# Kernel optimization log

Hardware: AMD Instinct MI355X
Metric: run time of the kernel (lower is better)

The kernel has to match this reference:

```python
import jax, jax.numpy as jnp
import numpy as np

NEG = -9.0e15


def setup_inputs() -> dict:
    key = jax.random.key(0)
    k_x, k_w, k_e, k_b, k_m = jax.random.split(key, 5)
    B, N, C, F = 2048, 64, 256, 256
    x = jax.random.normal(k_x, (B, N, C), dtype=jnp.float32)
    W = jax.random.normal(k_w, (2, C, F), dtype=jnp.float32) * (1.414 / np.sqrt(C + F))
    # full logit tensor; only entries where mask holds are ever read (equivalent
    # to torch's flat `e` scattered into the nonzero positions of adj)
    e = jax.random.normal(k_e, (F, N, N), dtype=jnp.float32)
    bias = jax.random.normal(k_b, (F,), dtype=jnp.float32) * (1.0 / np.sqrt(C))
    # symmetric adjacency mask with self-loops, density ~0.3
    m = jax.random.bernoulli(k_m, 0.3, (N, N))
    mask = (m | m.T) | jnp.eye(N, dtype=bool)
    return {"x": x, "W": W, "e": e, "bias": bias, "mask": mask}


def reference(x, W, e, bias, mask):
    # x: [B,N,C], W: [2,C,F], e: [F,N,N], bias: [F], mask: [N,N] bool
    h0 = x @ W[0]                                   # [B,N,F] (self term)
    h1 = x @ W[1]                                   # [B,N,F] (neighbor term)
    logits = jnp.where(mask[None, :, :], e, NEG)    # [F,N,N]
    adj = jax.nn.softmax(logits, axis=2)            # per-channel row softmax
    N = mask.shape[0]
    eye = jnp.eye(N, dtype=bool)
    d = jnp.diagonal(adj, axis1=1, axis2=2)         # [F,N]  (adj * E diagonal)
    off = jnp.where(eye[None, :, :], 0.0, adj)      # [F,N,N] (adj * (1-E))
    # (adj*E) @ h0 reduces to per-node diagonal scaling; off-diag is a
    # per-channel NxN matmul batched over B.
    out = d.T[None, :, :] * h0 + jnp.einsum('fnm,bmf->bnf', off, h1)
    return out + bias[None, None, :]
```

## Files before the change

kernel.cpp:

```cpp
#include <hip/hip_runtime.h>
#include <hip/hip_bf16.h>


typedef __attribute__((ext_vector_type(8))) short  fragA;
typedef __attribute__((ext_vector_type(4))) float  f32x4;
typedef __attribute__((ext_vector_type(8))) unsigned short u16x8;
typedef __attribute__((ext_vector_type(4))) unsigned short u16x4;

constexpr long OFF_OFF = 0;
constexpr long OFF_WT  = 2l * 1024 * 1024;
constexpr long OFF_DS  = OFF_WT + 512l * 256 * 2;
constexpr long WS_NEED = OFF_DS + 64l * 256 * 4;

static __device__ inline unsigned short f2bf(float f) {
  __hip_bfloat16 h = __float2bfloat16(f);
  return __builtin_bit_cast(unsigned short, h);
}
static __device__ inline float bf2f(unsigned short u) {
  unsigned int x = ((unsigned int)u) << 16;
  return __builtin_bit_cast(float, x);
}

__global__ __launch_bounds__(256) void k_prep(const float* __restrict__ e,
                                              const unsigned char* __restrict__ mask,
                                              char* __restrict__ ws_b) {
  unsigned short* off = (unsigned short*)(ws_b + OFF_OFF);
  float* dscale = (float*)(ws_b + OFF_DS);
  const int lane = threadIdx.x & 63;
  const int row  = blockIdx.x * 4 + (threadIdx.x >> 6);
  const int n = row & 63;

  bool is_u8 = __all(mask[lane * 65] != 0);
  bool mv;
  if (is_u8) mv = mask[n * 64 + lane] != 0;
  else       mv = ((const int*)mask)[n * 64 + lane] != 0;

  float v = mv ? e[(long)row * 64 + lane] : -1e30f;
  float mx = v;
#pragma unroll
  for (int s = 32; s; s >>= 1) mx = fmaxf(mx, __shfl_xor(mx, s));
  float ex = mv ? __expf(v - mx) : 0.f;
  float sm = ex;
#pragma unroll
  for (int s = 32; s; s >>= 1) sm += __shfl_xor(sm, s);
  float adj = ex / sm;
  const int f = row >> 6;
  if (lane == n) dscale[n * 256 + f] = adj;
  off[(long)row * 64 + lane] = f2bf(lane == n ? 0.f : adj);
}

__global__ __launch_bounds__(256) void k_wt(const float* __restrict__ W,
                                            char* __restrict__ ws_b) {
  unsigned short* Wt = (unsigned short*)(ws_b + OFF_WT);
  __shared__ float t[64][65];
  const int bid = blockIdx.x;
  const int w = bid >> 4, f0 = ((bid >> 2) & 3) * 64, c0 = (bid & 3) * 64;
  const int tr = threadIdx.x >> 2, tc = (threadIdx.x & 3) * 16;
  const float* src = W + ((long)(w * 256 + c0 + tr)) * 256 + f0 + tc;
#pragma unroll
  for (int i = 0; i < 16; i += 4) {
    float4 v = *(const float4*)(src + i);
    t[tr][tc + i] = v.x; t[tr][tc + i + 1] = v.y;
    t[tr][tc + i + 2] = v.z; t[tr][tc + i + 3] = v.w;
  }
  __syncthreads();
  u16x8 p0, p1;
#pragma unroll
  for (int i = 0; i < 8; i++)  p0[i] = f2bf(t[tc + i][tr]);
#pragma unroll
  for (int i = 0; i < 8; i++)  p1[i] = f2bf(t[tc + 8 + i][tr]);
  unsigned short* dst = Wt + ((long)(w * 256 + f0 + tr)) * 256 + c0 + tc;
  *(u16x8*)dst = p0;
  *(u16x8*)(dst + 8) = p1;
}

__global__ __launch_bounds__(512, 4) void k_main(const float* __restrict__ x,
                                                 const float* __restrict__ bias,
                                                 const char* __restrict__ ws_b,
                                                 float* __restrict__ out) {
  const unsigned short* Wt   = (const unsigned short*)(ws_b + OFF_WT);
  const unsigned short* offp = (const unsigned short*)(ws_b + OFF_OFF);
  const float* dscale        = (const float*)(ws_b + OFF_DS);

  __shared__ __align__(16) unsigned short Bs[64 * 264];
  __shared__ __align__(16) unsigned short Hb[19264];

  const int tid = threadIdx.x;
  const int wid = tid >> 6, lane = tid & 63;
  const int lr = lane & 15, hi = lane >> 4;

  const int wg = blockIdx.x;
  const int xcd = wg & 7, s = wg >> 3;
  const int bb = xcd * 32 + (s >> 3);
  const int fb = s & 7;
  const int f0 = fb * 32;
  const long R0 = (long)bb * 512;
  const long Rw = R0 + wid * 64;

  {
    int c = tid >> 3, ch = (tid & 7) * 32;
    int wrow = (c < 32) ? (f0 + c) : (256 + f0 + c - 32);
    const unsigned short* src = Wt + (long)wrow * 256 + ch;
    unsigned short* d = &Bs[c * 264 + ch];
    *(u16x8*)(d)      = *(const u16x8*)(src);
    *(u16x8*)(d + 8)  = *(const u16x8*)(src + 8);
    *(u16x8*)(d + 16) = *(const u16x8*)(src + 16);
    *(u16x8*)(d + 24) = *(const u16x8*)(src + 24);
  }
  __syncthreads();

  f32x4 acc[4][4] = {};
#pragma unroll
  for (int ks = 0; ks < 8; ks++) {
    fragA af[4], bfr[4];
#pragma unroll
    for (int i = 0; i < 4; i++) {
      const float* p = x + (Rw + i * 16 + lr) * 256 + ks * 32 + hi * 8;
      float4 v0 = *(const float4*)p;
      float4 v1 = *(const float4*)(p + 4);
      u16x8 t;
      t[0] = f2bf(v0.x); t[1] = f2bf(v0.y); t[2] = f2bf(v0.z); t[3] = f2bf(v0.w);
      t[4] = f2bf(v1.x); t[5] = f2bf(v1.y); t[6] = f2bf(v1.z); t[7] = f2bf(v1.w);
      af[i] = __builtin_bit_cast(fragA, t);
    }
#pragma unroll
    for (int j = 0; j < 4; j++)
      bfr[j] = *(const fragA*)&Bs[(j * 16 + lr) * 264 + ks * 32 + hi * 8];
#pragma unroll
    for (int i = 0; i < 4; i++)
#pragma unroll
      for (int j = 0; j < 4; j++)
        acc[i][j] = __builtin_amdgcn_mfma_f32_16x16x32_bf16(af[i], bfr[j], acc[i][j], 0, 0, 0);
  }

#pragma unroll
  for (int i = 0; i < 4; i++) {
#pragma unroll
    for (int j = 2; j < 4; j++) {
      int fl = (j - 2) * 16 + lr;
      int m  = i * 16 + hi * 4;
      u16x4 pk;
      pk[0] = f2bf(acc[i][j][0]); pk[1] = f2bf(acc[i][j][1]);
      pk[2] = f2bf(acc[i][j][2]); pk[3] = f2bf(acc[i][j][3]);
      *(u16x4*)&Hb[fl * 584 + wid * 72 + m] = pk;
    }
  }
  __syncthreads();

#pragma unroll
  for (int q = 0; q < 4; q++) {
    int fl = wid * 4 + q;
    long fg = f0 + fl;
    f32x4 ea[4] = {};
    const unsigned short* ob = offp + fg * 4096;
#pragma unroll
    for (int kk = 0; kk < 2; kk++) {
      fragA a = *(const fragA*)&Hb[fl * 584 + lr * 72 + kk * 32 + hi * 8];
#pragma unroll
      for (int ct = 0; ct < 4; ct++) {
        fragA b = *(const fragA*)(ob + (ct * 16 + lr) * 64 + kk * 32 + hi * 8);
        ea[ct] = __builtin_amdgcn_mfma_f32_16x16x32_bf16(a, b, ea[ct], 0, 0, 0);
      }
    }
    if (hi < 2) {
#pragma unroll
      for (int ct = 0; ct < 4; ct++) {
#pragma unroll
        for (int r = 0; r < 4; r++) {
          int b = hi * 4 + r;
          int n = ct * 16 + lr;
          Hb[fl * 584 + b * 72 + n] = f2bf(ea[ct][r]);
        }
      }
    }
  }
  __syncthreads();

#pragma unroll
  for (int i = 0; i < 4; i++) {
#pragma unroll
    for (int j = 0; j < 2; j++) {
      int fl = j * 16 + lr;
      int f  = f0 + fl;
      float bs = bias[f];
#pragma unroll
      for (int r = 0; r < 4; r++) {
        int m = i * 16 + hi * 4 + r;
        float ev = bf2f(Hb[fl * 584 + wid * 72 + m]);
        long R = Rw + m;
        out[R * 256 + f] = dscale[m * 256 + f] * acc[i][j][r] + ev + bs;
      }
    }
  }
}

extern "C" void kernel_launch(void* const* d_in, const int* in_sizes, int n_in,
                              void* d_out, int out_size, void* d_ws, size_t ws_size,
                              hipStream_t stream) {
  const float* x    = (const float*)d_in[0];
  const float* W    = (const float*)d_in[1];
  const float* e    = (const float*)d_in[2];
  const float* bias = (const float*)d_in[3];
  const unsigned char* mask = (const unsigned char*)d_in[4];
  float* out = (float*)d_out;
  char* ws = (char*)d_ws;
  if (ws_size < (size_t)WS_NEED) return;

  k_prep<<<4096, 256, 0, stream>>>(e, mask, ws);
  k_wt<<<32, 256, 0, stream>>>(W, ws);
  k_main<<<2048, 512, 0, stream>>>(x, bias, ws, out);
}
```

Before: 205.5 us.

## Pre-convert x to bf16 in a fused prep kernel and prefetch A fragments

Adds a bf16 copy of x in workspace, produced by a single merged prep kernel that also computes the softmax adjacency and transposed weights. The main kernel now reads bf16 x with register double-buffered prefetch, uses 256-thread blocks over twice as many row tiles, and the per-channel neighbor matmul uses only the needed rows. This removes in-loop fp32 loads and conversions and one launch, but adds an extra full pass writing and rereading x in bf16.

```diff
diff --git a/kernel.cpp b/kernel.cpp
--- a/kernel.cpp
+++ b/kernel.cpp
@@ -10,7 +10,8 @@
 constexpr long OFF_OFF = 0;
 constexpr long OFF_WT  = 2l * 1024 * 1024;
 constexpr long OFF_DS  = OFF_WT + 512l * 256 * 2;
-constexpr long WS_NEED = OFF_DS + 64l * 256 * 4;
+constexpr long OFF_XB  = OFF_DS + 64l * 256 * 4;
+constexpr long WS_NEED = OFF_XB + 131072l * 256 * 2;
 
 static __device__ inline unsigned short f2bf(float f) {
   __hip_bfloat16 h = __float2bfloat16(f);
@@ -21,116 +22,130 @@
   return __builtin_bit_cast(float, x);
 }
 
-__global__ __launch_bounds__(256) void k_prep(const float* __restrict__ e,
-                                              const unsigned char* __restrict__ mask,
-                                              char* __restrict__ ws_b) {
-  unsigned short* off = (unsigned short*)(ws_b + OFF_OFF);
-  float* dscale = (float*)(ws_b + OFF_DS);
-  const int lane = threadIdx.x & 63;
-  const int row  = blockIdx.x * 4 + (threadIdx.x >> 6);
-  const int n = row & 63;
-
-  bool is_u8 = __all(mask[lane * 65] != 0);
-  bool mv;
-  if (is_u8) mv = mask[n * 64 + lane] != 0;
-  else       mv = ((const int*)mask)[n * 64 + lane] != 0;
-
-  float v = mv ? e[(long)row * 64 + lane] : -1e30f;
-  float mx = v;
-#pragma unroll
-  for (int s = 32; s; s >>= 1) mx = fmaxf(mx, __shfl_xor(mx, s));
-  float ex = mv ? __expf(v - mx) : 0.f;
-  float sm = ex;
-#pragma unroll
-  for (int s = 32; s; s >>= 1) sm += __shfl_xor(sm, s);
-  float adj = ex / sm;
-  const int f = row >> 6;
-  if (lane == n) dscale[n * 256 + f] = adj;
-  off[(long)row * 64 + lane] = f2bf(lane == n ? 0.f : adj);
-}
-
-__global__ __launch_bounds__(256) void k_wt(const float* __restrict__ W,
-                                            char* __restrict__ ws_b) {
-  unsigned short* Wt = (unsigned short*)(ws_b + OFF_WT);
-  __shared__ float t[64][65];
+__global__ __launch_bounds__(256) void k_pre(const float* __restrict__ x,
+                                             const float* __restrict__ e,
+                                             const float* __restrict__ W,
+                                             const unsigned char* __restrict__ mask,
+                                             char* __restrict__ ws_b) {
   const int bid = blockIdx.x;
-  const int w = bid >> 4, f0 = ((bid >> 2) & 3) * 64, c0 = (bid & 3) * 64;
-  const int tr = threadIdx.x >> 2, tc = (threadIdx.x & 3) * 16;
-  const float* src = W + ((long)(w * 256 + c0 + tr)) * 256 + f0 + tc;
-#pragma unroll
-  for (int i = 0; i < 16; i += 4) {
-    float4 v = *(const float4*)(src + i);
-    t[tr][tc + i] = v.x; t[tr][tc + i + 1] = v.y;
-    t[tr][tc + i + 2] = v.z; t[tr][tc + i + 3] = v.w;
-  }
-  __syncthreads();
-  u16x8 p0, p1;
-#pragma unroll
-  for (int i = 0; i < 8; i++)  p0[i] = f2bf(t[tc + i][tr]);
-#pragma unroll
-  for (int i = 0; i < 8; i++)  p1[i] = f2bf(t[tc + 8 + i][tr]);
-  unsigned short* dst = Wt + ((long)(w * 256 + f0 + tr)) * 256 + c0 + tc;
-  *(u16x8*)dst = p0;
-  *(u16x8*)(dst + 8) = p1;
-}
-
-__global__ __launch_bounds__(512, 4) void k_main(const float* __restrict__ x,
-                                                 const float* __restrict__ bias,
+  const int tid = threadIdx.x;
+  if (bid < 4096) {
+    unsigned short* off = (unsigned short*)(ws_b + OFF_OFF);
+    float* dscale = (float*)(ws_b + OFF_DS);
+    const int lane = tid & 63;
+    const int row  = bid * 4 + (tid >> 6);
+    const int n = row & 63;
+    bool is_u8 = __all(mask[lane * 65] != 0);
+    bool mv;
+    if (is_u8) mv = mask[n * 64 + lane] != 0;
+    else       mv = ((const int*)mask)[n * 64 + lane] != 0;
+    float v = mv ? e[(long)row * 64 + lane] : -1e30f;
+    float mx = v;
+#pragma unroll
+    for (int s = 32; s; s >>= 1) mx = fmaxf(mx, __shfl_xor(mx, s));
+    float ex = mv ? __expf(v - mx) : 0.f;
+    float sm = ex;
+#pragma unroll
+    for (int s = 32; s; s >>= 1) sm += __shfl_xor(sm, s);
+    float adj = ex / sm;
+    const int f = row >> 6;
+    if (lane == n) dscale[n * 256 + f] = adj;
+    off[(long)row * 64 + lane] = f2bf(lane == n ? 0.f : adj);
+  } else if (bid < 6144) {
+    unsigned short* xb = (unsigned short*)(ws_b + OFF_XB);
+    long i = ((long)(bid - 4096) * 256 + tid) * 8;
+    const long stride = 2048l * 256 * 8;
+    const long total = 131072l * 256;
+    for (; i < total; i += stride) {
+      float4 a = *(const float4*)(x + i);
+      float4 b = *(const float4*)(x + i + 4);
+      u16x8 p;
+      p[0] = f2bf(a.x); p[1] = f2bf(a.y); p[2] = f2bf(a.z); p[3] = f2bf(a.w);
+      p[4] = f2bf(b.x); p[5] = f2bf(b.y); p[6] = f2bf(b.z); p[7] = f2bf(b.w);
+      *(u16x8*)(xb + i) = p;
+    }
+  } else {
+    unsigned short* Wt = (unsigned short*)(ws_b + OFF_WT);
+    __shared__ float t[64][65];
+    const int b2 = bid - 6144;
+    const int w = b2 >> 4, f0 = ((b2 >> 2) & 3) * 64, c0 = (b2 & 3) * 64;
+    const int tr = tid >> 2, tc = (tid & 3) * 16;
+    const float* src = W + ((long)(w * 256 + c0 + tr)) * 256 + f0 + tc;
+#pragma unroll
+    for (int i = 0; i < 16; i += 4) {
+      float4 v = *(const float4*)(src + i);
+      t[tr][tc + i] = v.x; t[tr][tc + i + 1] = v.y;
+      t[tr][tc + i + 2] = v.z; t[tr][tc + i + 3] = v.w;
+    }
+    __syncthreads();
+    u16x8 p0, p1;
+#pragma unroll
+    for (int i = 0; i < 8; i++)  p0[i] = f2bf(t[tc + i][tr]);
+#pragma unroll
+    for (int i = 0; i < 8; i++)  p1[i] = f2bf(t[tc + 8 + i][tr]);
+    unsigned short* dst = Wt + ((long)(w * 256 + f0 + tr)) * 256 + c0 + tc;
+    *(u16x8*)dst = p0;
+    *(u16x8*)(dst + 8) = p1;
+  }
+}
+
+__global__ __launch_bounds__(256, 3) void k_main(const float* __restrict__ bias,
                                                  const char* __restrict__ ws_b,
                                                  float* __restrict__ out) {
   const unsigned short* Wt   = (const unsigned short*)(ws_b + OFF_WT);
   const unsigned short* offp = (const unsigned short*)(ws_b + OFF_OFF);
+  const unsigned short* xb   = (const unsigned short*)(ws_b + OFF_XB);
   const float* dscale        = (const float*)(ws_b + OFF_DS);
 
   __shared__ __align__(16) unsigned short Bs[64 * 264];
-  __shared__ __align__(16) unsigned short Hb[19264];
+  __shared__ __align__(16) unsigned short Hb[32 * 296];
 
   const int tid = threadIdx.x;
   const int wid = tid >> 6, lane = tid & 63;
-  const int lr = lane & 15, hi = lane >> 4;
+  const int lr = lane & 15, qu = lane >> 4;
 
   const int wg = blockIdx.x;
   const int xcd = wg & 7, s = wg >> 3;
-  const int bb = xcd * 32 + (s >> 3);
+  const int bb = xcd * 64 + (s >> 3);
   const int fb = s & 7;
   const int f0 = fb * 32;
-  const long R0 = (long)bb * 512;
+  const long R0 = (long)bb * 256;
   const long Rw = R0 + wid * 64;
 
   {
-    int c = tid >> 3, ch = (tid & 7) * 32;
-    int wrow = (c < 32) ? (f0 + c) : (256 + f0 + c - 32);
-    const unsigned short* src = Wt + (long)wrow * 256 + ch;
-    unsigned short* d = &Bs[c * 264 + ch];
-    *(u16x8*)(d)      = *(const u16x8*)(src);
-    *(u16x8*)(d + 8)  = *(const u16x8*)(src + 8);
-    *(u16x8*)(d + 16) = *(const u16x8*)(src + 16);
-    *(u16x8*)(d + 24) = *(const u16x8*)(src + 24);
+    int col = tid & 63, kc = (tid >> 6) * 64;
+    int wrow = (col < 32) ? (f0 + col) : (256 + f0 + col - 32);
+    const unsigned short* src = Wt + (long)wrow * 256 + kc;
+    unsigned short* d = &Bs[col * 264 + kc];
+#pragma unroll
+    for (int i = 0; i < 8; i++)
+      *(u16x8*)(d + i * 8) = *(const u16x8*)(src + i * 8);
   }
   __syncthreads();
 
   f32x4 acc[4][4] = {};
+  const unsigned short* ax = xb + (Rw + lr) * 256 + qu * 8;
+  fragA a_cur[4], a_nxt[4];
+#pragma unroll
+  for (int i = 0; i < 4; i++) a_cur[i] = *(const fragA*)(ax + i * 4096);
 #pragma unroll
   for (int ks = 0; ks < 8; ks++) {
-    fragA af[4], bfr[4];
-#pragma unroll
-    for (int i = 0; i < 4; i++) {
-      const float* p = x + (Rw + i * 16 + lr) * 256 + ks * 32 + hi * 8;
-      float4 v0 = *(const float4*)p;
-      float4 v1 = *(const float4*)(p + 4);
-      u16x8 t;
-      t[0] = f2bf(v0.x); t[1] = f2bf(v0.y); t[2] = f2bf(v0.z); t[3] = f2bf(v0.w);
-      t[4] = f2bf(v1.x); t[5] = f2bf(v1.y); t[6] = f2bf(v1.z); t[7] = f2bf(v1.w);
-      af[i] = __builtin_bit_cast(fragA, t);
-    }
+    if (ks < 7) {
+#pragma unroll
+      for (int i = 0; i < 4; i++)
+        a_nxt[i] = *(const fragA*)(ax + i * 4096 + (ks + 1) * 32);
+    }
+    fragA bfr[4];
 #pragma unroll
     for (int j = 0; j < 4; j++)
-      bfr[j] = *(const fragA*)&Bs[(j * 16 + lr) * 264 + ks * 32 + hi * 8];
+      bfr[j] = *(const fragA*)&Bs[(j * 16 + lr) * 264 + ks * 32 + qu * 8];
 #pragma unroll
     for (int i = 0; i < 4; i++)
 #pragma unroll
       for (int j = 0; j < 4; j++)
-        acc[i][j] = __builtin_amdgcn_mfma_f32_16x16x32_bf16(af[i], bfr[j], acc[i][j], 0, 0, 0);
+        acc[i][j] = __builtin_amdgcn_mfma_f32_16x16x32_bf16(a_cur[i], bfr[j], acc[i][j], 0, 0, 0);
+#pragma unroll
+    for (int i = 0; i < 4; i++) a_cur[i] = a_nxt[i];
   }
 
 #pragma unroll
@@ -138,40 +153,39 @@
 #pragma unroll
     for (int j = 2; j < 4; j++) {
       int fl = (j - 2) * 16 + lr;
-      int m  = i * 16 + hi * 4;
+      int m  = i * 16 + qu * 4;
       u16x4 pk;
       pk[0] = f2bf(acc[i][j][0]); pk[1] = f2bf(acc[i][j][1]);
       pk[2] = f2bf(acc[i][j][2]); pk[3] = f2bf(acc[i][j][3]);
-      *(u16x4*)&Hb[fl * 584 + wid * 72 + m] = pk;
+      *(u16x4*)&Hb[fl * 296 + wid * 72 + m] = pk;
     }
   }
   __syncthreads();
 
-#pragma unroll
-  for (int q = 0; q < 4; q++) {
-    int fl = wid * 4 + q;
+  for (int q = 0; q < 8; q++) {
+    int fl = wid * 8 + q;
     long fg = f0 + fl;
+    const unsigned short* ob = offp + fg * 4096;
+    fragA a0 = *(const fragA*)&Hb[fl * 296 + (lr & 3) * 72 + qu * 8];
+    fragA a1 = *(const fragA*)&Hb[fl * 296 + (lr & 3) * 72 + 32 + qu * 8];
+    fragA b0[4], b1[4];
+#pragma unroll
+    for (int ct = 0; ct < 4; ct++) {
+      b0[ct] = *(const fragA*)(ob + (ct * 16 + lr) * 64 + qu * 8);
+      b1[ct] = *(const fragA*)(ob + (ct * 16 + lr) * 64 + 32 + qu * 8);
+    }
     f32x4 ea[4] = {};
-    const unsigned short* ob = offp + fg * 4096;
-#pragma unroll
-    for (int kk = 0; kk < 2; kk++) {
-      fragA a = *(const fragA*)&Hb[fl * 584 + lr * 72 + kk * 32 + hi * 8];
-#pragma unroll
-      for (int ct = 0; ct < 4; ct++) {
-        fragA b = *(const fragA*)(ob + (ct * 16 + lr) * 64 + kk * 32 + hi * 8);
-        ea[ct] = __builtin_amdgcn_mfma_f32_16x16x32_bf16(a, b, ea[ct], 0, 0, 0);
-      }
-    }
-    if (hi < 2) {
-#pragma unroll
-      for (int ct = 0; ct < 4; ct++) {
-#pragma unroll
-        for (int r = 0; r < 4; r++) {
-          int b = hi * 4 + r;
-          int n = ct * 16 + lr;
-          Hb[fl * 584 + b * 72 + n] = f2bf(ea[ct][r]);
-        }
-      }
+#pragma unroll
+    for (int ct = 0; ct < 4; ct++) {
+      ea[ct] = __builtin_amdgcn_mfma_f32_16x16x32_bf16(a0, b0[ct], ea[ct], 0, 0, 0);
+      ea[ct] = __builtin_amdgcn_mfma_f32_16x16x32_bf16(a1, b1[ct], ea[ct], 0, 0, 0);
+    }
+    if (qu == 0) {
+#pragma unroll
+      for (int ct = 0; ct < 4; ct++)
+#pragma unroll
+        for (int r = 0; r < 4; r++)
+          Hb[fl * 296 + r * 72 + ct * 16 + lr] = f2bf(ea[ct][r]);
     }
   }
   __syncthreads();
@@ -180,15 +194,14 @@
   for (int i = 0; i < 4; i++) {
 #pragma unroll
     for (int j = 0; j < 2; j++) {
-      int fl = j * 16 + lr;
-      int f  = f0 + fl;
+      int c = j * 16 + lr;
+      int f = f0 + c;
       float bs = bias[f];
 #pragma unroll
       for (int r = 0; r < 4; r++) {
-        int m = i * 16 + hi * 4 + r;
-        float ev = bf2f(Hb[fl * 584 + wid * 72 + m]);
-        long R = Rw + m;
-        out[R * 256 + f] = dscale[m * 256 + f] * acc[i][j][r] + ev + bs;
+        int m = i * 16 + qu * 4 + r;
+        float ev = bf2f(Hb[c * 296 + wid * 72 + m]);
+        out[(Rw + m) * 256 + f] = dscale[m * 256 + f] * acc[i][j][r] + ev + bs;
       }
     }
   }
@@ -206,7 +219,6 @@
   char* ws = (char*)d_ws;
   if (ws_size < (size_t)WS_NEED) return;
 
-  k_prep<<<4096, 256, 0, stream>>>(e, mask, ws);
-  k_wt<<<32, 256, 0, stream>>>(W, ws);
-  k_main<<<2048, 512, 0, stream>>>(x, bias, ws, out);
-}
+  k_pre<<<6176, 256, 0, stream>>>(x, e, W, mask, ws);
+  k_main<<<4096, 256, 0, stream>>>(bias, ws, out);
+}
```

New measurement: 239.7 us. 16.6% more time.
